# Kernel tuning notes

Hardware: AMD Instinct MI355X
Metric: run time of the kernel (lower is better)

The kernel has to match this reference:

```python
import jax, jax.numpy as jnp
import numpy as np

B, H, E = 16384, 4096, 64
TEMPERATURE = 1.0
SPARSITY = 0.8
K = max(1, int(E * (1.0 - SPARSITY)))  # = 12


def setup_inputs() -> dict:
    key = jax.random.key(0)
    k1, k2, k3, k4, k5 = jax.random.split(key, 5)
    std = 0.02
    return {
        "hidden_states": jax.random.normal(k1, (B, H), dtype=jnp.float32),
        "router_w": jax.random.normal(k2, (E, H), dtype=jnp.float32) * std,
        "sparsity_mask": jax.random.normal(k3, (E, H), dtype=jnp.float32) * std,
        "gate_w1": jax.random.normal(k4, (H // 2, H), dtype=jnp.float32) * std,
        "gate_b1": jnp.zeros((H // 2,), dtype=jnp.float32),
        "gate_w2": jax.random.normal(k5, (E, H // 2), dtype=jnp.float32) * std,
        "gate_b2": jnp.zeros((E,), dtype=jnp.float32),
    }


def reference(hidden_states, router_w, sparsity_mask, gate_w1, gate_b1, gate_w2, gate_b2):
    # gate network: Linear -> ReLU -> Linear -> Sigmoid
    h = jax.nn.relu(hidden_states @ gate_w1.T + gate_b1)          # [B, H/2]
    gates = jax.nn.sigmoid(h @ gate_w2.T + gate_b2)                # [B, E]
    # masked router projection
    masked_w = router_w * jax.nn.sigmoid(sparsity_mask)            # [E, H]
    router_logits = hidden_states @ masked_w.T                     # [B, E]
    scaled_logits = (router_logits * gates) / TEMPERATURE          # [B, E]
    # top-k selection + dual softmax
    top_k_logits, top_k_indices = jax.lax.top_k(scaled_logits, K)  # [B, K]
    expert_weights = jax.nn.softmax(top_k_logits, axis=-1)         # [B, K]
    probs = jax.nn.softmax(scaled_logits, axis=-1)                 # [B, E]
    # load-balancing stats
    expert_load = probs.mean(axis=0)                               # [E]
    load_variance = jnp.var(expert_load, ddof=1)                   # torch .var() is unbiased
    entropy = -(probs * jnp.log(probs + 1e-8)).sum(axis=-1).mean()
    return scaled_logits, top_k_indices, expert_weights, load_variance, entropy
```

## Files before the change

### kernel.cpp

```cpp
#include <hip/hip_runtime.h>

#define BROWS 16384
#define HDIM  4096
#define H2    2048
#define EEXP  64
#define KSEL  12

typedef float f32x4 __attribute__((ext_vector_type(4)));

__global__ void k_mw32(const float* __restrict__ rw, const float* __restrict__ mk,
                       float* __restrict__ mw, int n){
  int i = blockIdx.x*blockDim.x + threadIdx.x;
  if (i < n){
    float m = mk[i];
    float u = (float)exp(-(double)m);
    mw[i] = rw[i] * (1.0f/(1.0f + u));
  }
}

__global__ __launch_bounds__(256, 3)
void k_h128(const float* __restrict__ A, const float* __restrict__ B,
            float* __restrict__ C, const float* __restrict__ bias)
{
  __shared__ float As[32][132];
  __shared__ float Bs[32][132];
  const int t = threadIdx.x;
  const int w = t>>6, l = t&63;
  const int wr = w>>1, wc = w&1;
  const int ly = l>>3, lx = l&7;
  const int bid = blockIdx.x;
  const int qq = bid >> 3;
  const int mt = (bid & 7)*16 + (qq >> 4), nt = qq & 15;
  const long m0 = (long)mt*128; const int n0 = nt*128;
  const int myrow = wr*64 + ly*8;
  const int mycol = wc*64 + lx*8;
  const int sr = t>>1, sc = (t&1)*16;

  float acc[8][8] = {};
  const float* ap = A + (m0+sr)*(long)HDIM + sc;
  const float* bp = B + (size_t)(n0+sr)*HDIM + sc;

  f32x4 ar[4], br[4];
  auto gload = [&](int kb){
    #pragma unroll
    for (int u=0;u<4;u++){
      ar[u] = *(const f32x4*)(ap + kb + 4*u);
      br[u] = *(const f32x4*)(bp + kb + 4*u);
    }
  };
  gload(0);
  for (int kb = 0; kb < HDIM; kb += 32){
    __syncthreads();
    #pragma unroll
    for (int u=0;u<4;u++)
      #pragma unroll
      for (int v=0;v<4;v++){
        As[sc+4*u+v][sr] = ar[u][v];
        Bs[sc+4*u+v][sr] = br[u][v];
      }
    __syncthreads();
    if (kb + 32 < HDIM) gload(kb + 32);
    #pragma unroll 8
    for (int kk = 0; kk < 32; ++kk){
      f32x4 a0 = *(const f32x4*)&As[kk][myrow];
      f32x4 a1 = *(const f32x4*)&As[kk][myrow+4];
      f32x4 b0 = *(const f32x4*)&Bs[kk][mycol];
      f32x4 b1 = *(const f32x4*)&Bs[kk][mycol+4];
      #pragma unroll
      for (int j=0;j<8;j++){
        float bj = (j<4) ? b0[j] : b1[j-4];
        #pragma unroll
        for (int i=0;i<8;i++){
          float ai = (i<4) ? a0[i] : a1[i-4];
          acc[i][j] = fmaf(ai, bj, acc[i][j]);
        }
      }
    }
  }
  #pragma unroll
  for (int i=0;i<8;i++){
    const long row = m0 + myrow + i;
    f32x4 v0, v1;
    #pragma unroll
    for (int j=0;j<4;j++){
      v0[j] = fmaxf(acc[i][j]   + bias[n0+mycol+j],   0.f);
      v1[j] = fmaxf(acc[i][j+4] + bias[n0+mycol+4+j], 0.f);
    }
    *(f32x4*)&C[row*(long)H2 + n0 + mycol]     = v0;
    *(f32x4*)&C[row*(long)H2 + n0 + mycol + 4] = v1;
  }
}

__global__ __launch_bounds__(256, 2)
void k_g32(const float* __restrict__ A, const float* __restrict__ B,
           float* __restrict__ C, int K, int ntiles,
           const float* __restrict__ bias, int relu)
{
  __shared__ float As[64][36];
  __shared__ float Bs[64][36];
  const int t = threadIdx.x;
  const int mt = blockIdx.x / ntiles, nt = blockIdx.x % ntiles;
  const long m0 = (long)mt*64; const int n0 = nt*64;
  const int ty = t>>4, tx = t&15;
  const int sr = t>>2, sc = (t&3)*8;
  float acc[4][4] = {{0.f,0.f,0.f,0.f},{0.f,0.f,0.f,0.f},
                     {0.f,0.f,0.f,0.f},{0.f,0.f,0.f,0.f}};
  const float* ap = A + (m0+sr)*(long)K + sc;
  const float* bp = B + ((size_t)(n0+sr))*K + sc;
  f32x4 a0,a1,b0,b1;
  auto gload = [&](int kb){
    a0 = *(const f32x4*)(ap + kb);
    a1 = *(const f32x4*)(ap + kb + 4);
    b0 = *(const f32x4*)(bp + kb);
    b1 = *(const f32x4*)(bp + kb + 4);
  };
  gload(0);
  for (int kb = 0; kb < K; kb += 32){
    __syncthreads();
    *(f32x4*)&As[sr][sc]   = a0; *(f32x4*)&As[sr][sc+4] = a1;
    *(f32x4*)&Bs[sr][sc]   = b0; *(f32x4*)&Bs[sr][sc+4] = b1;
    __syncthreads();
    if (kb + 32 < K) gload(kb + 32);
    #pragma unroll
    for (int kk = 0; kk < 32; kk += 4){
      f32x4 av[4], bv[4];
      #pragma unroll
      for (int i=0;i<4;i++) av[i] = *(const f32x4*)&As[ty+16*i][kk];
      #pragma unroll
      for (int j=0;j<4;j++) bv[j] = *(const f32x4*)&Bs[tx+16*j][kk];
      #pragma unroll
      for (int q=0;q<4;q++)
        #pragma unroll
        for (int i=0;i<4;i++)
          #pragma unroll
          for (int j=0;j<4;j++)
            acc[i][j] = fmaf(av[i][q], bv[j][q], acc[i][j]);
    }
  }
  #pragma unroll
  for (int i=0;i<4;i++){
    const long row = m0 + ty + 16*i;
    #pragma unroll
    for (int j=0;j<4;j++){
      const int col = n0 + tx + 16*j;
      float v = acc[i][j];
      if (bias) v = v + bias[col];
      if (relu) v = fmaxf(v, 0.f);
      C[row*(long)(ntiles*64) + col] = v;
    }
  }
}

__global__ void k_sig(const float* __restrict__ z, const float* __restrict__ rl,
                      const float* __restrict__ b2, float* __restrict__ s,
                      float* __restrict__ out0, int n){
  int i = blockIdx.x*blockDim.x + threadIdx.x;
  if (i < n){
    int e = i & (EEXP-1);
    float zz = z[i] + b2[e];
    float u = (float)exp(-(double)zz);
    float g = 1.0f/(1.0f + u);
    float sv = rl[i] * g;
    s[i] = sv;
    out0[i] = sv;
  }
}

__global__ __launch_bounds__(256, 2)
void k_top(const float* __restrict__ s32, float* __restrict__ out,
           float* __restrict__ loadp, float* __restrict__ entp)
{
  __shared__ float P[256][65];
  __shared__ float entbuf[256];
  const int t = threadIdx.x;
  const long row = (long)blockIdx.x*256 + t;
  const float* srow = s32 + row*EEXP;

  float vals[KSEL]; int idxs[KSEL];
  float pv = INFINITY; int pi = -1;
  for (int kk=0; kk<KSEL; ++kk){
    float bv = -INFINITY; int bi = 0;
    for (int e=0; e<EEXP; ++e){
      float v = srow[e];
      bool after = (v < pv) || ((v == pv) && (e > pi));
      if (after && (v > bv)){ bv = v; bi = e; }
    }
    vals[kk] = bv; idxs[kk] = bi; pv = bv; pi = bi;
  }
  float* oi = out + (size_t)BROWS*EEXP;
  float* ow = oi + (size_t)BROWS*KSEL;
  const long obase = row*KSEL;
  {
    float ev[KSEL]; float sw = 0.f;
    #pragma unroll
    for (int kk=0; kk<KSEL; ++kk){ ev[kk] = expf(vals[kk]-vals[0]); sw += ev[kk]; }
    float inv = 1.f/sw;
    #pragma unroll
    for (int kk=0; kk<KSEL; ++kk){ oi[obase+kk] = (float)idxs[kk]; ow[obase+kk] = ev[kk]*inv; }
  }
  {
    float mx = vals[0];
    float sum = 0.f;
    for (int e=0; e<EEXP; ++e) sum += expf(srow[e] - mx);
    float isum = 1.f/sum, ent = 0.f;
    for (int e=0; e<EEXP; ++e){
      float p2 = expf(srow[e] - mx) * isum;
      ent -= p2 * logf(p2 + 1e-8f);
      P[t][e] = p2;
    }
    entbuf[t] = ent;
  }
  __syncthreads();
  if (t < 64){
    float s = 0.f;
    for (int r2=0; r2<256; ++r2) s += P[r2][t];
    loadp[blockIdx.x*64 + t] = s;
    float es = entbuf[t] + entbuf[t+64] + entbuf[t+128] + entbuf[t+192];
    for (int o=32; o; o>>=1) es += __shfl_down(es, o);
    if (t == 0) entp[blockIdx.x] = es;
  }
}

__global__ void k_finalize(const float* __restrict__ loadp, const float* __restrict__ entp,
                           float* __restrict__ out){
  const int e = threadIdx.x;
  float s = 0.f;
  for (int b=0; b<64; ++b) s += loadp[b*64 + e];
  float load = s * (1.f/16384.f);
  float tsum = load;
  for (int o=32; o; o>>=1) tsum += __shfl_xor(tsum, o);
  float mean = tsum * (1.f/64.f);
  float d = load - mean;
  float v = d*d;
  for (int o=32; o; o>>=1) v += __shfl_xor(v, o);
  float var = v * (1.f/63.f);
  float es = entp[e];
  for (int o=32; o; o>>=1) es += __shfl_xor(es, o);
  if (e == 0){
    size_t off = (size_t)BROWS*EEXP + (size_t)BROWS*KSEL*2;
    out[off]     = var;
    out[off + 1] = es * (1.f/16384.f);
  }
}

extern "C" void kernel_launch(void* const* d_in, const int* in_sizes, int n_in,
                              void* d_out, int out_size, void* d_ws, size_t ws_size,
                              hipStream_t stream)
{
  const float* hidden = (const float*)d_in[0];
  const float* rw     = (const float*)d_in[1];
  const float* mk     = (const float*)d_in[2];
  const float* gw1    = (const float*)d_in[3];
  const float* gb1    = (const float*)d_in[4];
  const float* gw2    = (const float*)d_in[5];
  const float* gb2    = (const float*)d_in[6];
  float* out = (float*)d_out;

  unsigned char* ws = (unsigned char*)d_ws;
  size_t o = 0;
  float* mw  = (float*)(ws + o); o += (size_t)EEXP*HDIM*4;
  float* h   = (float*)(ws + o); o += (size_t)BROWS*H2*4;
  float* rl  = (float*)(ws + o); o += (size_t)BROWS*EEXP*4;
  float* zb  = (float*)(ws + o); o += (size_t)BROWS*EEXP*4;
  float* s32 = (float*)(ws + o); o += (size_t)BROWS*EEXP*4;
  float* loadp = (float*)(ws + o); o += 64*64*4;
  float* entp  = (float*)(ws + o); o += 256;

  k_mw32<<<(EEXP*HDIM+255)/256, 256, 0, stream>>>(rw, mk, mw, EEXP*HDIM);
  k_h128<<<(BROWS/128)*(H2/128), 256, 0, stream>>>(hidden, gw1, h, gb1);
  k_g32<<<(BROWS/64)*1, 256, 0, stream>>>(hidden, mw, rl, HDIM, 1, nullptr, 0);
  k_g32<<<(BROWS/64)*1, 256, 0, stream>>>(h, gw2, zb, H2, 1, nullptr, 0);
  k_sig<<<(BROWS*EEXP+255)/256, 256, 0, stream>>>(zb, rl, gb2, s32, out, BROWS*EEXP);
  k_top<<<BROWS/256, 256, 0, stream>>>(s32, out, loadp, entp);
  k_finalize<<<1, 64, 0, stream>>>(loadp, entp, out);
}
```

Before: 3.551 ms.

## Transpose GEMM operands and stream K-major tiles via direct global-to-LDS loads

Adds a transpose kernel that writes hidden_states and gate_w1 into K-major copies in workspace. A new FP32 GEMM kernel then fills double-buffered LDS tiles with global_load_lds DMA and overlaps the next tile's load with the current tile's FMA compute. This removes the per-thread register staging and strided loads of the old kernel. The cost is roughly 300 MB of extra transpose traffic, a larger workspace requirement, and a fallback to the old kernel when the workspace is too small.

```diff
diff --git a/kernel.cpp b/kernel.cpp
--- a/kernel.cpp
+++ b/kernel.cpp
@@ -7,6 +7,13 @@
 #define KSEL  12
 
 typedef float f32x4 __attribute__((ext_vector_type(4)));
+
+typedef __attribute__((address_space(1))) const unsigned int guint_t;
+typedef __attribute__((address_space(3))) unsigned int luint_t;
+
+__device__ __forceinline__ void gl16(const void* g, void* l){
+  __builtin_amdgcn_global_load_lds((guint_t*)g, (luint_t*)l, 16, 0, 0);
+}
 
 __global__ void k_mw32(const float* __restrict__ rw, const float* __restrict__ mk,
                        float* __restrict__ mw, int n){
@@ -15,6 +22,100 @@
     float m = mk[i];
     float u = (float)exp(-(double)m);
     mw[i] = rw[i] * (1.0f/(1.0f + u));
+  }
+}
+
+__global__ __launch_bounds__(256)
+void k_tr(const float* __restrict__ in, float* __restrict__ out, int R, int C){
+  __shared__ float tile[32][33];
+  const int t = threadIdx.x;
+  const int cb = C >> 5;
+  const int bx = blockIdx.x % cb, by = blockIdx.x / cb;
+  const int lr = t >> 3, lc4 = (t & 7) * 4;
+  f32x4 v = *(const f32x4*)(in + (size_t)(by*32 + lr)*C + bx*32 + lc4);
+  tile[lr][lc4] = v[0]; tile[lr][lc4+1] = v[1];
+  tile[lr][lc4+2] = v[2]; tile[lr][lc4+3] = v[3];
+  __syncthreads();
+  f32x4 o;
+  o[0] = tile[lc4][lr]; o[1] = tile[lc4+1][lr];
+  o[2] = tile[lc4+2][lr]; o[3] = tile[lc4+3][lr];
+  *(f32x4*)(out + (size_t)(bx*32 + lr)*R + by*32 + lc4) = o;
+}
+
+__global__ __launch_bounds__(256, 2)
+void k_hdd(const float* __restrict__ Atr, const float* __restrict__ Btr,
+           const float* __restrict__ bias, float* __restrict__ C)
+{
+  __shared__ float As[2][16][128];
+  __shared__ float Bs[2][16][128];
+  const int t = threadIdx.x, w = t>>6, l = t&63;
+  const int ly = l>>3, lx = l&7;
+  const int bid = blockIdx.x;
+  const int qq = bid >> 3;
+  const int mt = (bid & 7)*16 + (qq >> 4), nt = qq & 15;
+  const long m0 = (long)mt*128; const int n0 = nt*128;
+  const int r0 = (w>>1)*64 + ly*8;
+  const int c0 = (w&1)*64 + lx*8;
+
+  float acc[8][8] = {};
+
+  const float* agA = Atr + m0 + (size_t)(l>>5)*BROWS + (size_t)(l&31)*4;
+  const float* agB = Btr + n0 + (size_t)(l>>5)*H2   + (size_t)(l&31)*4;
+
+  auto dma = [&](int p, int buf){
+    const int kb = p*16;
+    #pragma unroll
+    for (int i=0;i<2;i++){
+      const int kk = 4*w + 2*i;
+      gl16(agA + (size_t)(kb+kk)*BROWS, &As[buf][kk][0]);
+      gl16(agB + (size_t)(kb+kk)*H2,   &Bs[buf][kk][0]);
+    }
+  };
+
+  auto compute = [&](int buf){
+    #pragma unroll
+    for (int kk=0; kk<16; ++kk){
+      f32x4 a0 = *(const f32x4*)&As[buf][kk][r0];
+      f32x4 a1 = *(const f32x4*)&As[buf][kk][r0+4];
+      f32x4 b0 = *(const f32x4*)&Bs[buf][kk][c0];
+      f32x4 b1 = *(const f32x4*)&Bs[buf][kk][c0+4];
+      #pragma unroll
+      for (int i=0;i<4;i++)
+        #pragma unroll
+        for (int j=0;j<4;j++){
+          acc[i][j]     = fmaf(a0[i], b0[j], acc[i][j]);
+          acc[i][j+4]   = fmaf(a0[i], b1[j], acc[i][j+4]);
+          acc[i+4][j]   = fmaf(a1[i], b0[j], acc[i+4][j]);
+          acc[i+4][j+4] = fmaf(a1[i], b1[j], acc[i+4][j+4]);
+        }
+    }
+  };
+
+  dma(0, 0);
+  asm volatile("s_waitcnt vmcnt(0)" ::: "memory");
+  __syncthreads();
+
+  for (int p = 0; p < 256; ++p){
+    const int buf = p & 1;
+    if (p + 1 < 256) dma(p+1, buf^1);
+    compute(buf);
+    asm volatile("s_waitcnt vmcnt(0)" ::: "memory");
+    __syncthreads();
+  }
+
+  const float* bp = bias + n0 + c0;
+  f32x4 bv0 = *(const f32x4*)bp, bv1 = *(const f32x4*)(bp+4);
+  #pragma unroll
+  for (int i=0;i<8;i++){
+    const long row = m0 + r0 + i;
+    f32x4 v0, v1;
+    #pragma unroll
+    for (int j=0;j<4;j++){
+      v0[j] = fmaxf(acc[i][j]   + bv0[j], 0.f);
+      v1[j] = fmaxf(acc[i][j+4] + bv1[j], 0.f);
+    }
+    *(f32x4*)&C[row*(long)H2 + n0 + c0]     = v0;
+    *(f32x4*)&C[row*(long)H2 + n0 + c0 + 4] = v1;
   }
 }
 
@@ -265,9 +366,20 @@
   float* s32 = (float*)(ws + o); o += (size_t)BROWS*EEXP*4;
   float* loadp = (float*)(ws + o); o += 64*64*4;
   float* entp  = (float*)(ws + o); o += 256;
+  float* Btr = (float*)(ws + o); o += (size_t)HDIM*H2*4;
+  float* Atr = (float*)(ws + o); o += (size_t)HDIM*BROWS*4;
+  const size_t need_full = o;
 
   k_mw32<<<(EEXP*HDIM+255)/256, 256, 0, stream>>>(rw, mk, mw, EEXP*HDIM);
-  k_h128<<<(BROWS/128)*(H2/128), 256, 0, stream>>>(hidden, gw1, h, gb1);
+
+  if (ws_size >= need_full){
+    k_tr<<<(HDIM/32)*(H2/32),    256, 0, stream>>>(gw1,    Btr, H2,    HDIM);
+    k_tr<<<(HDIM/32)*(BROWS/32), 256, 0, stream>>>(hidden, Atr, BROWS, HDIM);
+    k_hdd<<<(BROWS/128)*(H2/128), 256, 0, stream>>>(Atr, Btr, gb1, h);
+  } else {
+    k_h128<<<(BROWS/128)*(H2/128), 256, 0, stream>>>(hidden, gw1, h, gb1);
+  }
+
   k_g32<<<(BROWS/64)*1, 256, 0, stream>>>(hidden, mw, rl, HDIM, 1, nullptr, 0);
   k_g32<<<(BROWS/64)*1, 256, 0, stream>>>(h, gw2, zb, H2, 1, nullptr, 0);
   k_sig<<<(BROWS*EEXP+255)/256, 256, 0, stream>>>(zb, rl, gb2, s32, out, BROWS*EEXP);
```

New measurement: 3.781 ms. +6.5%, slower.
